# Kernel tuning notes

Measured on AMD Instinct MI355X. Metric: run time of the kernel, lower is better.

The kernel has to match this reference:

```python
import jax, jax.numpy as jnp
import numpy as np
import math

D_MODEL = 768
N_HEADS = 12
B, L = 2, 2048
ALPHA = 0.3

def setup_inputs() -> dict:
    key = jax.random.key(0)
    ks = jax.random.split(key, 7)
    s = 0.02
    return {
        "x": jax.random.normal(ks[0], (B, L, D_MODEL), dtype=jnp.float32),
        "Wqkv_w": jax.random.normal(ks[1], (D_MODEL, 3 * D_MODEL), dtype=jnp.float32) * s,
        "Wqkv_b": jax.random.normal(ks[2], (3 * D_MODEL,), dtype=jnp.float32) * s,
        "sel_w": jax.random.normal(ks[3], (D_MODEL, 2), dtype=jnp.float32) * s,
        "sel_b": jax.random.normal(ks[4], (2,), dtype=jnp.float32) * s,
        "out_w": jax.random.normal(ks[5], (D_MODEL, D_MODEL), dtype=jnp.float32) * s,
        "out_b": jax.random.normal(ks[6], (D_MODEL,), dtype=jnp.float32) * s,
        "temperature": jnp.ones((1,), dtype=jnp.float32) * (math.sqrt(D_MODEL) * ALPHA),
    }

def reference(x, Wqkv_w, Wqkv_b, sel_w, sel_b, out_w, out_b, temperature):
    b, l, d = x.shape
    h = N_HEADS
    hd = d // h
    # QKV projection: (B, L, 3, H, hd)
    qkv = (x @ Wqkv_w + Wqkv_b).reshape(b, l, 3, h, hd)
    q, k_, v = qkv[:, :, 0], qkv[:, :, 1], qkv[:, :, 2]
    scale = 1.0 / math.sqrt(hd)
    scores = jnp.einsum('bthd,bshd->bhts', q, k_ * scale)  # (B,H,L,L)
    causal_mask = jnp.triu(jnp.full((l, l), -10000.0, dtype=scores.dtype), 1)
    attn = jax.nn.softmax(scores + causal_mask, axis=-1)
    ctx = jnp.einsum('bhts,bshd->bthd', attn, v).reshape(b, l, d)
    attn_output = ctx @ out_w + out_b  # (B,L,D)
    # selection gate: softmax over 2 logits, keep prob of class 1 -> (B,L,1)
    selection = jax.nn.softmax((x @ sel_w + sel_b) / temperature, axis=-1)[..., 1:]
    # eval-mode top-k routing
    k_sel = int(math.ceil(math.sqrt(l)))
    _, idx = jax.lax.top_k(selection[..., 0], k_sel)  # (B, k)
    gated = attn_output * selection  # (B,L,D)
    src = jnp.take_along_axis(gated, idx[..., None], axis=1)  # (B,k,D)
    y = jax.vmap(lambda xb, ib, sb: xb.at[ib].add(sb))(x, idx, src)
    return y
```

## Files before the change

### kernel.cpp

```cpp
#include <hip/hip_runtime.h>
#include <hip/hip_bf16.h>
#include <cstddef>

#define BATCH 2
#define SEQ   2048
#define DM    768
#define NH    12
#define HD    64
#define N3    2304
#define NKV   1536
#define KSEL  46
#define NROW  (BATCH*KSEL)
#define NCHUNK 32

typedef unsigned short ushort_t;
typedef __attribute__((ext_vector_type(8))) short bf16x8;
typedef __attribute__((ext_vector_type(4))) float f32x4;

__device__ __forceinline__ ushort_t f2bf(float f) {
  union { __hip_bfloat16 h; ushort_t u; } cv;
  cv.h = __float2bfloat16(f);
  return cv.u;
}
__device__ __forceinline__ float bf2f(ushort_t u) {
  union { unsigned int i; float f; } cv;
  cv.i = ((unsigned int)u) << 16;
  return cv.f;
}

#define GLD16(g, l)                                                         \
  __builtin_amdgcn_global_load_lds(                                         \
      (const __attribute__((address_space(1))) void*)(g),                   \
      (__attribute__((address_space(3))) void*)(l), 16, 0, 0)

__global__ __launch_bounds__(256) void prep_kernel(
    const float* __restrict__ x, const float* __restrict__ W,
    const float* __restrict__ Wo,
    const float* __restrict__ sel_w, const float* __restrict__ sel_b,
    const float* __restrict__ temp,
    ushort_t* __restrict__ xb, ushort_t* __restrict__ Wt,
    ushort_t* __restrict__ WoT,
    float* __restrict__ sel, float* __restrict__ y) {
  const int bx = blockIdx.x;
  const int tid = threadIdx.x;
  if (bx < 1024) {
    const int w = tid >> 6, lane = tid & 63;
    const int row = bx * 4 + w;
    const float4* xr4 = (const float4*)(x + (size_t)row * DM);
    float4* yr4 = (float4*)(y + (size_t)row * DM);
    ushort4* xb4 = (ushort4*)(xb + (size_t)row * DM);
    const float4* sw4 = (const float4*)sel_w;
    float a0 = 0.f, a1 = 0.f;
#pragma unroll
    for (int i = 0; i < 3; ++i) {
      const int p = i * 64 + lane;
      float4 f = xr4[p];
      yr4[p] = f;
      ushort4 o;
      o.x = f2bf(f.x); o.y = f2bf(f.y); o.z = f2bf(f.z); o.w = f2bf(f.w);
      xb4[p] = o;
      float4 sa = sw4[p * 2];
      float4 sb = sw4[p * 2 + 1];
      a0 += f.x * sa.x + f.y * sa.z + f.z * sb.x + f.w * sb.z;
      a1 += f.x * sa.y + f.y * sa.w + f.z * sb.y + f.w * sb.w;
    }
    for (int off = 32; off; off >>= 1) {
      a0 += __shfl_xor(a0, off);
      a1 += __shfl_xor(a1, off);
    }
    if (lane == 0) {
      float t = temp[0];
      float l0 = (a0 + sel_b[0]) / t;
      float l1 = (a1 + sel_b[1]) / t;
      sel[row] = 1.0f / (1.0f + expf(l0 - l1));
    }
  } else if (bx < 2752) {
    __shared__ float tile[32][33];
    const int bx2 = bx - 1024;
    const int n0 = (bx2 % 72) * 32, k0 = (bx2 / 72) * 32;
    const int r = tid >> 3, c4 = (tid & 7) * 4;
    float4 f = *(const float4*)&W[(size_t)(k0 + r) * N3 + n0 + c4];
    tile[r][c4] = f.x; tile[r][c4 + 1] = f.y; tile[r][c4 + 2] = f.z; tile[r][c4 + 3] = f.w;
    __syncthreads();
    ushort4 o;
    o.x = f2bf(tile[c4 + 0][r]);
    o.y = f2bf(tile[c4 + 1][r]);
    o.z = f2bf(tile[c4 + 2][r]);
    o.w = f2bf(tile[c4 + 3][r]);
    *(ushort4*)&Wt[(size_t)(n0 + r) * DM + k0 + c4] = o;
  } else {
    __shared__ float tile2[32][33];
    const int bx3 = bx - 2752;
    const int n0 = (bx3 % 24) * 32, k0 = (bx3 / 24) * 32;
    const int r = tid >> 3, c4 = (tid & 7) * 4;
    float4 f = *(const float4*)&Wo[(size_t)(k0 + r) * DM + n0 + c4];
    tile2[r][c4] = f.x; tile2[r][c4 + 1] = f.y; tile2[r][c4 + 2] = f.z; tile2[r][c4 + 3] = f.w;
    __syncthreads();
    ushort4 o;
    o.x = f2bf(tile2[c4 + 0][r]);
    o.y = f2bf(tile2[c4 + 1][r]);
    o.z = f2bf(tile2[c4 + 2][r]);
    o.w = f2bf(tile2[c4 + 3][r]);
    *(ushort4*)&WoT[(size_t)(n0 + r) * DM + k0 + c4] = o;
  }
}

__global__ __launch_bounds__(256) void topk_kernel(
    const float* __restrict__ sel, int* __restrict__ idx,
    int* __restrict__ idxp) {
  __shared__ unsigned int hist[256];
  __shared__ unsigned int cum[256];
  __shared__ unsigned int wtot[4];
  __shared__ int sh_b;
  __shared__ int c_gt, c_eq;
  __shared__ int tmp_gt[KSEL];
  __shared__ int eqlist[256];
  const int b = blockIdx.x, tid = threadIdx.x;
  const int lane = tid & 63, w = tid >> 6;

  unsigned int key[8];
  int  kidx[8];
#pragma unroll
  for (int e = 0; e < 8; ++e) {
    int i = e * 256 + tid;
    kidx[e] = i;
    key[e] = __float_as_uint(sel[b * SEQ + i]);
  }
  unsigned int prefix = 0, mask = 0;
  int r = KSEL;
#pragma unroll
  for (int p = 3; p >= 0; --p) {
    const int shift = 8 * p;
    hist[tid] = 0;
    __syncthreads();
#pragma unroll
    for (int e = 0; e < 8; ++e)
      if ((key[e] & mask) == prefix)
        atomicAdd(&hist[(key[e] >> shift) & 255], 1u);
    __syncthreads();
    unsigned int v = hist[tid];
#pragma unroll
    for (int off = 1; off < 64; off <<= 1) {
      unsigned int t = __shfl_down(v, off);
      if (lane + off < 64) v += t;
    }
    if (lane == 0) wtot[w] = v;
    __syncthreads();
    unsigned int addhi = 0;
    for (int ww = w + 1; ww < 4; ++ww) addhi += wtot[ww];
    v += addhi;
    cum[tid] = v;
    __syncthreads();
    if (v >= (unsigned int)r && (tid == 255 || cum[tid + 1] < (unsigned int)r))
      sh_b = tid;
    __syncthreads();
    const int bsel = sh_b;
    r -= (bsel == 255) ? 0 : (int)cum[bsel + 1];
    prefix |= ((unsigned int)bsel) << shift;
    mask |= 0xFFu << shift;
    __syncthreads();
  }
  if (tid == 0) { c_gt = 0; c_eq = 0; }
  __syncthreads();
#pragma unroll
  for (int e = 0; e < 8; ++e) {
    if (key[e] > prefix) {
      int pos = atomicAdd(&c_gt, 1);
      tmp_gt[pos] = kidx[e];
    } else if (key[e] == prefix) {
      int pos = atomicAdd(&c_eq, 1);
      if (pos < 256) eqlist[pos] = kidx[e];
    }
  }
  __syncthreads();
  if (tid == 0) {
    const int need = KSEL - c_gt;
    const int ec = (c_eq < 256) ? c_eq : 256;
    for (int a = 0; a < need; ++a) {
      int mb = a;
      for (int bb = a + 1; bb < ec; ++bb)
        if (eqlist[bb] < eqlist[mb]) mb = bb;
      int tv = eqlist[a]; eqlist[a] = eqlist[mb]; eqlist[mb] = tv;
    }
  }
  __syncthreads();
  if (tid < 64) {
    if (tid < KSEL) {
      int t = (tid < c_gt) ? tmp_gt[tid] : eqlist[tid - c_gt];
      idx[b * KSEL + tid] = t;
      idxp[b * 64 + tid] = t;
    } else {
      idxp[b * 64 + tid] = 0;
    }
  }
}

__global__ __launch_bounds__(256) void gemm_kernel(
    const ushort_t* __restrict__ Xbf,
    const ushort_t* __restrict__ Wt,
    const float* __restrict__ bias,
    const int* __restrict__ idxp,
    ushort_t* __restrict__ Ckv,
    ushort_t* __restrict__ qb) {
  __shared__ ushort_t As[128 * 32];
  __shared__ ushort_t Bs[128 * 32];
  const int bid = blockIdx.x;
  const int tid = threadIdx.x;
  const int lane = tid & 63, w = tid >> 6;
  const int wr = w >> 1, wc = w & 1;
  const int quad = lane >> 4, l16 = lane & 15;
  const int ci0 = tid;
  const int ci1 = 256 + tid;
  const bool isQ = (bid >= 384);
  int m0, n0;
  size_t ga0, ga1;
  if (isQ) {
    m0 = 0;
    n0 = (bid - 384) * 128;
    const int r0 = ci0 >> 2, r1 = ci1 >> 2;
    ga0 = (size_t)((r0 >> 6) * SEQ + idxp[r0]) * DM;
    ga1 = (size_t)((r1 >> 6) * SEQ + idxp[r1]) * DM;
  } else {
    m0 = (bid / 12) * 128;
    n0 = 768 + (bid % 12) * 128;
    ga0 = (size_t)(m0 + (ci0 >> 2)) * DM;
    ga1 = (size_t)(m0 + (ci1 >> 2)) * DM;
  }
  const size_t gb0 = (size_t)(n0 + (ci0 >> 2)) * DM;
  const size_t gb1 = (size_t)(n0 + (ci1 >> 2)) * DM;
  const int ka0 = (ci0 & 3) * 8, ka1 = (ci1 & 3) * 8;

  f32x4 acc[4][4] = {};
  for (int k0 = 0; k0 < DM; k0 += 32) {
    GLD16(Xbf + ga0 + k0 + ka0, &As[(w * 64) * 8]);
    GLD16(Xbf + ga1 + k0 + ka1, &As[(256 + w * 64) * 8]);
    GLD16(Wt + gb0 + k0 + ka0, &Bs[(w * 64) * 8]);
    GLD16(Wt + gb1 + k0 + ka1, &Bs[(256 + w * 64) * 8]);
    __syncthreads();
    bf16x8 af[4], bfr[4];
#pragma unroll
    for (int i = 0; i < 4; ++i)
      af[i] = *(const bf16x8*)&As[(wr * 64 + i * 16 + l16) * 32 + quad * 8];
#pragma unroll
    for (int j = 0; j < 4; ++j)
      bfr[j] = *(const bf16x8*)&Bs[(wc * 64 + j * 16 + l16) * 32 + quad * 8];
#pragma unroll
    for (int i = 0; i < 4; ++i)
#pragma unroll
      for (int j = 0; j < 4; ++j)
        acc[i][j] = __builtin_amdgcn_mfma_f32_16x16x32_bf16(af[i], bfr[j], acc[i][j], 0, 0, 0);
    __syncthreads();
  }
#pragma unroll
  for (int i = 0; i < 4; ++i) {
    const int row_base = wr * 64 + i * 16 + quad * 4;
#pragma unroll
    for (int j = 0; j < 4; ++j) {
      const int col = n0 + wc * 64 + j * 16 + l16;
      const float bv = bias[col];
      if (isQ) {
#pragma unroll
        for (int r = 0; r < 4; ++r)
          qb[(size_t)(row_base + r) * DM + col] = f2bf(acc[i][j][r] + bv);
      } else {
#pragma unroll
        for (int r = 0; r < 4; ++r)
          Ckv[(size_t)(m0 + row_base + r) * NKV + (col - 768)] = f2bf(acc[i][j][r] + bv);
      }
    }
  }
}

__global__ __launch_bounds__(256) void attn_chunk_kernel(
    const ushort_t* __restrict__ kv,
    const ushort_t* __restrict__ qb,
    const int* __restrict__ idx,
    float* __restrict__ m_part, float* __restrict__ l_part,
    ushort_t* __restrict__ o_part) {
  __shared__ __align__(16) ushort_t Vt[64][72];
  __shared__ __align__(16) ushort_t Ps[4][16][72];
  __shared__ int tS[64];
  __shared__ int tmaxS;
  const int tid = threadIdx.x;
  const int c = blockIdx.x, h = blockIdx.y, b = blockIdx.z;
  const int c0 = c * 64;
  if (tid < 64) {
    int t = (tid < KSEL) ? idx[b * KSEL + tid] : -1;
    tS[tid] = t;
    int tm = t;
    for (int off = 32; off; off >>= 1) tm = max(tm, __shfl_xor(tm, off));
    if (tid == 0) tmaxS = tm;
  }
  __syncthreads();
  if (c0 > tmaxS) return;

  {
    const int key = tid >> 2, ds0 = (tid & 3) * 16;
    const ushort_t* vsrc = kv + (size_t)(b * SEQ + c0 + key) * NKV + DM + h * HD + ds0;
    ushort_t tmp[16];
    *(uint4*)&tmp[0] = *(const uint4*)&vsrc[0];
    *(uint4*)&tmp[8] = *(const uint4*)&vsrc[8];
#pragma unroll
    for (int i = 0; i < 16; ++i) Vt[ds0 + i][key] = tmp[i];
  }

  const int lane = tid & 63, w = tid >> 6;
  const int quad = lane >> 4, l16 = lane & 15;

  const ushort_t* qsrc = qb + (size_t)(b * 64 + w * 16 + l16) * DM + h * HD + quad * 8;
  bf16x8 aq0 = *(const bf16x8*)&qsrc[0];
  bf16x8 aq1 = *(const bf16x8*)&qsrc[32];

  f32x4 acc[4] = {};
#pragma unroll
  for (int nt = 0; nt < 4; ++nt) {
    const ushort_t* ksrc = kv + (size_t)(b * SEQ + c0 + nt * 16 + l16) * NKV + h * HD + quad * 8;
    bf16x8 bk0 = *(const bf16x8*)&ksrc[0];
    bf16x8 bk1 = *(const bf16x8*)&ksrc[32];
    acc[nt] = __builtin_amdgcn_mfma_f32_16x16x32_bf16(aq0, bk0, acc[nt], 0, 0, 0);
    acc[nt] = __builtin_amdgcn_mfma_f32_16x16x32_bf16(aq1, bk1, acc[nt], 0, 0, 0);
  }

  float p[4][4];
  float mrow[4], lrow[4];
#pragma unroll
  for (int r = 0; r < 4; ++r) {
    const int q = w * 16 + quad * 4 + r;
    const int t = tS[q];
    float mx = -1e30f;
#pragma unroll
    for (int nt = 0; nt < 4; ++nt) {
      float s = acc[nt][r] * 0.125f;
      if (c0 + nt * 16 + l16 > t) s = -1e30f;
      p[nt][r] = s;
      mx = fmaxf(mx, s);
    }
#pragma unroll
    for (int off = 1; off < 16; off <<= 1) mx = fmaxf(mx, __shfl_xor(mx, off));
    float sum = 0.f;
#pragma unroll
    for (int nt = 0; nt < 4; ++nt) {
      float pv = __expf(p[nt][r] - mx);
      p[nt][r] = pv;
      sum += pv;
    }
#pragma unroll
    for (int off = 1; off < 16; off <<= 1) sum += __shfl_xor(sum, off);
    mrow[r] = mx; lrow[r] = sum;
  }

  const size_t pbase = ((size_t)(b * NH + h) * NCHUNK + c) * 64;
  if (l16 == 0) {
#pragma unroll
    for (int r = 0; r < 4; ++r) {
      const int q = w * 16 + quad * 4 + r;
      m_part[pbase + q] = mrow[r];
      l_part[pbase + q] = lrow[r];
    }
  }

#pragma unroll
  for (int r = 0; r < 4; ++r)
#pragma unroll
    for (int nt = 0; nt < 4; ++nt)
      Ps[w][quad * 4 + r][nt * 16 + l16] = f2bf(p[nt][r]);
  __syncthreads();

  bf16x8 ap0 = *(const bf16x8*)&Ps[w][l16][quad * 8];
  bf16x8 ap1 = *(const bf16x8*)&Ps[w][l16][32 + quad * 8];
  f32x4 acc2[4] = {};
#pragma unroll
  for (int nt = 0; nt < 4; ++nt) {
    bf16x8 bv0 = *(const bf16x8*)&Vt[nt * 16 + l16][quad * 8];
    bf16x8 bv1 = *(const bf16x8*)&Vt[nt * 16 + l16][32 + quad * 8];
    acc2[nt] = __builtin_amdgcn_mfma_f32_16x16x32_bf16(ap0, bv0, acc2[nt], 0, 0, 0);
    acc2[nt] = __builtin_amdgcn_mfma_f32_16x16x32_bf16(ap1, bv1, acc2[nt], 0, 0, 0);
  }
  ushort_t* obp = o_part + pbase * 64;
#pragma unroll
  for (int nt = 0; nt < 4; ++nt)
#pragma unroll
    for (int r = 0; r < 4; ++r)
      obp[(w * 16 + quad * 4 + r) * 64 + nt * 16 + l16] = f2bf(acc2[nt][r]);
}

__global__ __launch_bounds__(256) void attn_combine_kernel(
    const float* __restrict__ m_part, const float* __restrict__ l_part,
    const ushort_t* __restrict__ o_part, const int* __restrict__ idx,
    ushort_t* __restrict__ ctx_bf) {
  __shared__ float wgt[NCHUNK][16];
  __shared__ float linv[16];
  __shared__ int ncS[16];
  const int rg = blockIdx.x, h = blockIdx.y, b = blockIdx.z;
  const int tid = threadIdx.x;
  const size_t base = (size_t)(b * NH + h) * NCHUNK * 64;
  if (tid < 16) {
    const int q = rg * 16 + tid;
    float L = 0.f; int nc = 0;
    if (q < KSEL) {
      const int t = idx[b * KSEL + q];
      nc = (t >> 6) + 1;
      float M = -1e30f;
      for (int cc = 0; cc < nc; ++cc)
        M = fmaxf(M, m_part[base + cc * 64 + q]);
      for (int cc = 0; cc < nc; ++cc) {
        float wv = __expf(m_part[base + cc * 64 + q] - M);
        wgt[cc][tid] = wv;
        L += wv * l_part[base + cc * 64 + q];
      }
    }
    ncS[tid] = nc;
    linv[tid] = (L > 0.f) ? 1.0f / L : 0.f;
  }
  __syncthreads();
  const int rl = tid >> 4;
  const int d4 = (tid & 15) * 4;
  const int q = rg * 16 + rl;
  if (q >= KSEL) return;
  const int nc = ncS[rl];
  float4 a = {0.f, 0.f, 0.f, 0.f};
  const ushort_t* obp = o_part + base * 64 + (size_t)q * 64 + d4;
  for (int cc = 0; cc < nc; ++cc) {
    const float wv = wgt[cc][rl];
    const ushort4 ov = *(const ushort4*)&obp[(size_t)cc * 4096];
    a.x += wv * bf2f(ov.x); a.y += wv * bf2f(ov.y);
    a.z += wv * bf2f(ov.z); a.w += wv * bf2f(ov.w);
  }
  const float li = linv[rl];
  ushort4 o;
  o.x = f2bf(a.x * li); o.y = f2bf(a.y * li);
  o.z = f2bf(a.z * li); o.w = f2bf(a.w * li);
  *(ushort4*)&ctx_bf[(size_t)(b * 64 + q) * DM + h * HD + d4] = o;
}

__global__ __launch_bounds__(256) void outproj_kernel(
    const ushort_t* __restrict__ ctx_bf,
    const ushort_t* __restrict__ WoT,
    const float* __restrict__ ob, const int* __restrict__ idx,
    const float* __restrict__ sel, float* __restrict__ y) {
  __shared__ ushort_t As[128 * 32];
  __shared__ ushort_t Bs[64 * 32];
  const int tid = threadIdx.x;
  const int lane = tid & 63, w = tid >> 6;
  const int wr = w >> 1, wc = w & 1;
  const int kb = blockIdx.x / 12;
  const int n0 = (blockIdx.x % 12) * 64;
  const int kbase = kb * 384;
  const int quad = lane >> 4, l16 = lane & 15;
  const int ci0 = tid;
  const int ci1 = 256 + tid;
  const size_t ga0 = (size_t)(ci0 >> 2) * DM;
  const size_t ga1 = (size_t)(ci1 >> 2) * DM;
  const size_t gb0 = (size_t)(n0 + (tid >> 2)) * DM;
  const int ka0 = (ci0 & 3) * 8, ka1 = (ci1 & 3) * 8;
  const int kq = (tid & 3) * 8;
  f32x4 acc[4][2] = {};
  for (int k0 = kbase; k0 < kbase + 384; k0 += 32) {
    GLD16(ctx_bf + ga0 + k0 + ka0, &As[(w * 64) * 8]);
    GLD16(ctx_bf + ga1 + k0 + ka1, &As[(256 + w * 64) * 8]);
    GLD16(WoT + gb0 + k0 + kq, &Bs[(w * 16) * 32]);
    __syncthreads();
    bf16x8 af[4], bfr[2];
#pragma unroll
    for (int i = 0; i < 4; ++i)
      af[i] = *(const bf16x8*)&As[(wr * 64 + i * 16 + l16) * 32 + quad * 8];
#pragma unroll
    for (int j = 0; j < 2; ++j)
      bfr[j] = *(const bf16x8*)&Bs[(wc * 32 + j * 16 + l16) * 32 + quad * 8];
#pragma unroll
    for (int i = 0; i < 4; ++i)
#pragma unroll
      for (int j = 0; j < 2; ++j)
        acc[i][j] = __builtin_amdgcn_mfma_f32_16x16x32_bf16(af[i], bfr[j], acc[i][j], 0, 0, 0);
    __syncthreads();
  }
#pragma unroll
  for (int i = 0; i < 4; ++i) {
#pragma unroll
    for (int r = 0; r < 4; ++r) {
      const int row = wr * 64 + i * 16 + quad * 4 + r;
      const int b = row >> 6, jj = row & 63;
      if (jj >= KSEL) continue;
      const int t = idx[b * KSEL + jj];
      const float sv = sel[b * SEQ + t];
      float* yr = y + (size_t)(b * SEQ + t) * DM;
#pragma unroll
      for (int j = 0; j < 2; ++j) {
        const int col = n0 + wc * 32 + j * 16 + l16;
        const float bv = (kb == 0) ? ob[col] : 0.f;
        atomicAdd(&yr[col], (acc[i][j][r] + bv) * sv);
      }
    }
  }
}

extern "C" void kernel_launch(void* const* d_in, const int* in_sizes, int n_in,
                              void* d_out, int out_size, void* d_ws, size_t ws_size,
                              hipStream_t stream) {
  const float* x      = (const float*)d_in[0];
  const float* Wqkv_w = (const float*)d_in[1];
  const float* Wqkv_b = (const float*)d_in[2];
  const float* sel_w  = (const float*)d_in[3];
  const float* sel_b  = (const float*)d_in[4];
  const float* out_w  = (const float*)d_in[5];
  const float* out_b  = (const float*)d_in[6];
  const float* temp   = (const float*)d_in[7];
  float* y = (float*)d_out;

  char* wsb = (char*)d_ws;
  ushort_t* kv     = (ushort_t*)wsb;  wsb += (size_t)BATCH * SEQ * NKV * 2;
  ushort_t* o_part = (ushort_t*)wsb;  wsb += (size_t)24 * NCHUNK * 64 * 64 * 2;
  float*    m_part = (float*)wsb;     wsb += (size_t)24 * NCHUNK * 64 * 4;
  float*    l_part = (float*)wsb;     wsb += (size_t)24 * NCHUNK * 64 * 4;
  float*    sel    = (float*)wsb;     wsb += (size_t)BATCH * SEQ * 4;
  int*      idx    = (int*)wsb;       wsb += 128 * 4;
  int*      idxp   = (int*)wsb;       wsb += 128 * 4;
  ushort_t* ctx_bf = (ushort_t*)wsb;  wsb += (size_t)128 * DM * 2;
  ushort_t* qb     = (ushort_t*)wsb;  wsb += (size_t)128 * DM * 2;
  ushort_t* Xbf    = (ushort_t*)wsb;  wsb += (size_t)BATCH * SEQ * DM * 2;
  ushort_t* Wt     = (ushort_t*)wsb;  wsb += (size_t)N3 * DM * 2;
  ushort_t* WoT    = (ushort_t*)wsb;  wsb += (size_t)DM * DM * 2;

  prep_kernel<<<dim3(3328), 256, 0, stream>>>(x, Wqkv_w, out_w, sel_w, sel_b, temp,
                                              Xbf, Wt, WoT, sel, y);
  topk_kernel<<<dim3(BATCH), 256, 0, stream>>>(sel, idx, idxp);
  gemm_kernel<<<dim3(390), 256, 0, stream>>>(Xbf, Wt, Wqkv_b, idxp, kv, qb);
  attn_chunk_kernel<<<dim3(NCHUNK, NH, BATCH), 256, 0, stream>>>(kv, qb, idx, m_part, l_part, o_part);
  attn_combine_kernel<<<dim3(3, NH, BATCH), 256, 0, stream>>>(m_part, l_part, o_part, idx, ctx_bf);
  outproj_kernel<<<dim3(24), 256, 0, stream>>>(ctx_bf, WoT, out_b, idx, sel, y);
}
```

Measured before the change: 154.8 us.

## Fuse top-k into Q-GEMM blocks and attention combine into chunk kernel

The separate top-k kernel is removed. Each of the six Q-projection GEMM blocks now recomputes the radix-select top-k for both batches itself and keeps the indices in shared memory, and block 384 writes idx for later kernels. The attention combine kernel is folded into the chunk kernel: a per-(batch,head) atomic counter, zeroed in the prep kernel, lets the last finishing chunk block merge the partial results. This removes two kernel launches and their serialization gaps, at the cost of redundant top-k work in the Q blocks, which delays them, and a serial combine tail run by one block per head.

```diff
diff --git a/kernel.cpp b/kernel.cpp
--- a/kernel.cpp
+++ b/kernel.cpp
@@ -40,10 +40,12 @@
     const float* __restrict__ temp,
     ushort_t* __restrict__ xb, ushort_t* __restrict__ Wt,
     ushort_t* __restrict__ WoT,
-    float* __restrict__ sel, float* __restrict__ y) {
+    float* __restrict__ sel, float* __restrict__ y,
+    unsigned int* __restrict__ cnt) {
   const int bx = blockIdx.x;
   const int tid = threadIdx.x;
   if (bx < 1024) {
+    if (bx == 0 && tid < NH * BATCH) cnt[tid] = 0u;
     const int w = tid >> 6, lane = tid & 63;
     const int row = bx * 4 + w;
     const float4* xr4 = (const float4*)(x + (size_t)row * DM);
@@ -105,105 +107,24 @@
   }
 }
 
-__global__ __launch_bounds__(256) void topk_kernel(
-    const float* __restrict__ sel, int* __restrict__ idx,
-    int* __restrict__ idxp) {
+__global__ __launch_bounds__(256) void gemm_kernel(
+    const ushort_t* __restrict__ Xbf,
+    const ushort_t* __restrict__ Wt,
+    const float* __restrict__ bias,
+    const float* __restrict__ sel,
+    int* __restrict__ idx,
+    ushort_t* __restrict__ Ckv,
+    ushort_t* __restrict__ qb) {
+  __shared__ ushort_t As[128 * 32];
+  __shared__ ushort_t Bs[128 * 32];
   __shared__ unsigned int hist[256];
-  __shared__ unsigned int cum[256];
+  __shared__ unsigned int cumS[256];
   __shared__ unsigned int wtot[4];
   __shared__ int sh_b;
   __shared__ int c_gt, c_eq;
   __shared__ int tmp_gt[KSEL];
   __shared__ int eqlist[256];
-  const int b = blockIdx.x, tid = threadIdx.x;
-  const int lane = tid & 63, w = tid >> 6;
-
-  unsigned int key[8];
-  int  kidx[8];
-#pragma unroll
-  for (int e = 0; e < 8; ++e) {
-    int i = e * 256 + tid;
-    kidx[e] = i;
-    key[e] = __float_as_uint(sel[b * SEQ + i]);
-  }
-  unsigned int prefix = 0, mask = 0;
-  int r = KSEL;
-#pragma unroll
-  for (int p = 3; p >= 0; --p) {
-    const int shift = 8 * p;
-    hist[tid] = 0;
-    __syncthreads();
-#pragma unroll
-    for (int e = 0; e < 8; ++e)
-      if ((key[e] & mask) == prefix)
-        atomicAdd(&hist[(key[e] >> shift) & 255], 1u);
-    __syncthreads();
-    unsigned int v = hist[tid];
-#pragma unroll
-    for (int off = 1; off < 64; off <<= 1) {
-      unsigned int t = __shfl_down(v, off);
-      if (lane + off < 64) v += t;
-    }
-    if (lane == 0) wtot[w] = v;
-    __syncthreads();
-    unsigned int addhi = 0;
-    for (int ww = w + 1; ww < 4; ++ww) addhi += wtot[ww];
-    v += addhi;
-    cum[tid] = v;
-    __syncthreads();
-    if (v >= (unsigned int)r && (tid == 255 || cum[tid + 1] < (unsigned int)r))
-      sh_b = tid;
-    __syncthreads();
-    const int bsel = sh_b;
-    r -= (bsel == 255) ? 0 : (int)cum[bsel + 1];
-    prefix |= ((unsigned int)bsel) << shift;
-    mask |= 0xFFu << shift;
-    __syncthreads();
-  }
-  if (tid == 0) { c_gt = 0; c_eq = 0; }
-  __syncthreads();
-#pragma unroll
-  for (int e = 0; e < 8; ++e) {
-    if (key[e] > prefix) {
-      int pos = atomicAdd(&c_gt, 1);
-      tmp_gt[pos] = kidx[e];
-    } else if (key[e] == prefix) {
-      int pos = atomicAdd(&c_eq, 1);
-      if (pos < 256) eqlist[pos] = kidx[e];
-    }
-  }
-  __syncthreads();
-  if (tid == 0) {
-    const int need = KSEL - c_gt;
-    const int ec = (c_eq < 256) ? c_eq : 256;
-    for (int a = 0; a < need; ++a) {
-      int mb = a;
-      for (int bb = a + 1; bb < ec; ++bb)
-        if (eqlist[bb] < eqlist[mb]) mb = bb;
-      int tv = eqlist[a]; eqlist[a] = eqlist[mb]; eqlist[mb] = tv;
-    }
-  }
-  __syncthreads();
-  if (tid < 64) {
-    if (tid < KSEL) {
-      int t = (tid < c_gt) ? tmp_gt[tid] : eqlist[tid - c_gt];
-      idx[b * KSEL + tid] = t;
-      idxp[b * 64 + tid] = t;
-    } else {
-      idxp[b * 64 + tid] = 0;
-    }
-  }
-}
-
-__global__ __launch_bounds__(256) void gemm_kernel(
-    const ushort_t* __restrict__ Xbf,
-    const ushort_t* __restrict__ Wt,
-    const float* __restrict__ bias,
-    const int* __restrict__ idxp,
-    ushort_t* __restrict__ Ckv,
-    ushort_t* __restrict__ qb) {
-  __shared__ ushort_t As[128 * 32];
-  __shared__ ushort_t Bs[128 * 32];
+  __shared__ int idxp_s[128];
   const int bid = blockIdx.x;
   const int tid = threadIdx.x;
   const int lane = tid & 63, w = tid >> 6;
@@ -215,11 +136,88 @@
   int m0, n0;
   size_t ga0, ga1;
   if (isQ) {
+    for (int bb = 0; bb < 2; ++bb) {
+      unsigned int key[8];
+      int kidx[8];
+#pragma unroll
+      for (int e = 0; e < 8; ++e) {
+        int i = e * 256 + tid;
+        kidx[e] = i;
+        key[e] = __float_as_uint(sel[bb * SEQ + i]);
+      }
+      unsigned int prefix = 0, msk = 0;
+      int rr = KSEL;
+#pragma unroll
+      for (int p = 3; p >= 0; --p) {
+        const int shift = 8 * p;
+        hist[tid] = 0;
+        __syncthreads();
+#pragma unroll
+        for (int e = 0; e < 8; ++e)
+          if ((key[e] & msk) == prefix)
+            atomicAdd(&hist[(key[e] >> shift) & 255], 1u);
+        __syncthreads();
+        unsigned int v = hist[tid];
+#pragma unroll
+        for (int off = 1; off < 64; off <<= 1) {
+          unsigned int t = __shfl_down(v, off);
+          if (lane + off < 64) v += t;
+        }
+        if (lane == 0) wtot[w] = v;
+        __syncthreads();
+        unsigned int addhi = 0;
+        for (int ww = w + 1; ww < 4; ++ww) addhi += wtot[ww];
+        v += addhi;
+        cumS[tid] = v;
+        __syncthreads();
+        if (v >= (unsigned int)rr && (tid == 255 || cumS[tid + 1] < (unsigned int)rr))
+          sh_b = tid;
+        __syncthreads();
+        const int bsel = sh_b;
+        rr -= (bsel == 255) ? 0 : (int)cumS[bsel + 1];
+        prefix |= ((unsigned int)bsel) << shift;
+        msk |= 0xFFu << shift;
+        __syncthreads();
+      }
+      if (tid == 0) { c_gt = 0; c_eq = 0; }
+      __syncthreads();
+#pragma unroll
+      for (int e = 0; e < 8; ++e) {
+        if (key[e] > prefix) {
+          int pos = atomicAdd(&c_gt, 1);
+          tmp_gt[pos] = kidx[e];
+        } else if (key[e] == prefix) {
+          int pos = atomicAdd(&c_eq, 1);
+          if (pos < 256) eqlist[pos] = kidx[e];
+        }
+      }
+      __syncthreads();
+      if (tid == 0) {
+        const int need = KSEL - c_gt;
+        const int ec = (c_eq < 256) ? c_eq : 256;
+        for (int a = 0; a < need; ++a) {
+          int mb = a;
+          for (int b2 = a + 1; b2 < ec; ++b2)
+            if (eqlist[b2] < eqlist[mb]) mb = b2;
+          int tv = eqlist[a]; eqlist[a] = eqlist[mb]; eqlist[mb] = tv;
+        }
+      }
+      __syncthreads();
+      if (tid < 64) {
+        int t = 0;
+        if (tid < KSEL) {
+          t = (tid < c_gt) ? tmp_gt[tid] : eqlist[tid - c_gt];
+          if (bid == 384) idx[bb * KSEL + tid] = t;
+        }
+        idxp_s[bb * 64 + tid] = t;
+      }
+      __syncthreads();
+    }
     m0 = 0;
     n0 = (bid - 384) * 128;
     const int r0 = ci0 >> 2, r1 = ci1 >> 2;
-    ga0 = (size_t)((r0 >> 6) * SEQ + idxp[r0]) * DM;
-    ga1 = (size_t)((r1 >> 6) * SEQ + idxp[r1]) * DM;
+    ga0 = (size_t)((r0 >> 6) * SEQ + idxp_s[r0]) * DM;
+    ga1 = (size_t)((r1 >> 6) * SEQ + idxp_s[r1]) * DM;
   } else {
     m0 = (bid / 12) * 128;
     n0 = 768 + (bid % 12) * 128;
@@ -276,11 +274,17 @@
     const ushort_t* __restrict__ qb,
     const int* __restrict__ idx,
     float* __restrict__ m_part, float* __restrict__ l_part,
-    ushort_t* __restrict__ o_part) {
+    ushort_t* __restrict__ o_part,
+    unsigned int* __restrict__ cnt,
+    ushort_t* __restrict__ ctx_bf) {
   __shared__ __align__(16) ushort_t Vt[64][72];
   __shared__ __align__(16) ushort_t Ps[4][16][72];
   __shared__ int tS[64];
   __shared__ int tmaxS;
+  __shared__ float wgt[NCHUNK][16];
+  __shared__ float linv[16];
+  __shared__ int ncS[16];
+  __shared__ unsigned int oldS;
   const int tid = threadIdx.x;
   const int c = blockIdx.x, h = blockIdx.y, b = blockIdx.z;
   const int c0 = c * 64;
@@ -292,145 +296,146 @@
     if (tid == 0) tmaxS = tm;
   }
   __syncthreads();
-  if (c0 > tmaxS) return;
-
-  {
-    const int key = tid >> 2, ds0 = (tid & 3) * 16;
-    const ushort_t* vsrc = kv + (size_t)(b * SEQ + c0 + key) * NKV + DM + h * HD + ds0;
-    ushort_t tmp[16];
-    *(uint4*)&tmp[0] = *(const uint4*)&vsrc[0];
-    *(uint4*)&tmp[8] = *(const uint4*)&vsrc[8];
-#pragma unroll
-    for (int i = 0; i < 16; ++i) Vt[ds0 + i][key] = tmp[i];
-  }
-
-  const int lane = tid & 63, w = tid >> 6;
-  const int quad = lane >> 4, l16 = lane & 15;
-
-  const ushort_t* qsrc = qb + (size_t)(b * 64 + w * 16 + l16) * DM + h * HD + quad * 8;
-  bf16x8 aq0 = *(const bf16x8*)&qsrc[0];
-  bf16x8 aq1 = *(const bf16x8*)&qsrc[32];
-
-  f32x4 acc[4] = {};
-#pragma unroll
-  for (int nt = 0; nt < 4; ++nt) {
-    const ushort_t* ksrc = kv + (size_t)(b * SEQ + c0 + nt * 16 + l16) * NKV + h * HD + quad * 8;
-    bf16x8 bk0 = *(const bf16x8*)&ksrc[0];
-    bf16x8 bk1 = *(const bf16x8*)&ksrc[32];
-    acc[nt] = __builtin_amdgcn_mfma_f32_16x16x32_bf16(aq0, bk0, acc[nt], 0, 0, 0);
-    acc[nt] = __builtin_amdgcn_mfma_f32_16x16x32_bf16(aq1, bk1, acc[nt], 0, 0, 0);
-  }
-
-  float p[4][4];
-  float mrow[4], lrow[4];
-#pragma unroll
-  for (int r = 0; r < 4; ++r) {
-    const int q = w * 16 + quad * 4 + r;
-    const int t = tS[q];
-    float mx = -1e30f;
+
+  if (c0 <= tmaxS) {
+    {
+      const int key = tid >> 2, ds0 = (tid & 3) * 16;
+      const ushort_t* vsrc = kv + (size_t)(b * SEQ + c0 + key) * NKV + DM + h * HD + ds0;
+      ushort_t tmp[16];
+      *(uint4*)&tmp[0] = *(const uint4*)&vsrc[0];
+      *(uint4*)&tmp[8] = *(const uint4*)&vsrc[8];
+#pragma unroll
+      for (int i = 0; i < 16; ++i) Vt[ds0 + i][key] = tmp[i];
+    }
+
+    const int lane = tid & 63, w = tid >> 6;
+    const int quad = lane >> 4, l16 = lane & 15;
+
+    const ushort_t* qsrc = qb + (size_t)(b * 64 + w * 16 + l16) * DM + h * HD + quad * 8;
+    bf16x8 aq0 = *(const bf16x8*)&qsrc[0];
+    bf16x8 aq1 = *(const bf16x8*)&qsrc[32];
+
+    f32x4 acc[4] = {};
 #pragma unroll
     for (int nt = 0; nt < 4; ++nt) {
-      float s = acc[nt][r] * 0.125f;
-      if (c0 + nt * 16 + l16 > t) s = -1e30f;
-      p[nt][r] = s;
-      mx = fmaxf(mx, s);
-    }
-#pragma unroll
-    for (int off = 1; off < 16; off <<= 1) mx = fmaxf(mx, __shfl_xor(mx, off));
-    float sum = 0.f;
-#pragma unroll
-    for (int nt = 0; nt < 4; ++nt) {
-      float pv = __expf(p[nt][r] - mx);
-      p[nt][r] = pv;
-      sum += pv;
-    }
-#pragma unroll
-    for (int off = 1; off < 16; off <<= 1) sum += __shfl_xor(sum, off);
-    mrow[r] = mx; lrow[r] = sum;
-  }
-
-  const size_t pbase = ((size_t)(b * NH + h) * NCHUNK + c) * 64;
-  if (l16 == 0) {
+      const ushort_t* ksrc = kv + (size_t)(b * SEQ + c0 + nt * 16 + l16) * NKV + h * HD + quad * 8;
+      bf16x8 bk0 = *(const bf16x8*)&ksrc[0];
+      bf16x8 bk1 = *(const bf16x8*)&ksrc[32];
+      acc[nt] = __builtin_amdgcn_mfma_f32_16x16x32_bf16(aq0, bk0, acc[nt], 0, 0, 0);
+      acc[nt] = __builtin_amdgcn_mfma_f32_16x16x32_bf16(aq1, bk1, acc[nt], 0, 0, 0);
+    }
+
+    float p[4][4];
+    float mrow[4], lrow[4];
 #pragma unroll
     for (int r = 0; r < 4; ++r) {
       const int q = w * 16 + quad * 4 + r;
-      m_part[pbase + q] = mrow[r];
-      l_part[pbase + q] = lrow[r];
-    }
-  }
-
-#pragma unroll
-  for (int r = 0; r < 4; ++r)
+      const int t = tS[q];
+      float mx = -1e30f;
+#pragma unroll
+      for (int nt = 0; nt < 4; ++nt) {
+        float s = acc[nt][r] * 0.125f;
+        if (c0 + nt * 16 + l16 > t) s = -1e30f;
+        p[nt][r] = s;
+        mx = fmaxf(mx, s);
+      }
+#pragma unroll
+      for (int off = 1; off < 16; off <<= 1) mx = fmaxf(mx, __shfl_xor(mx, off));
+      float sum = 0.f;
+#pragma unroll
+      for (int nt = 0; nt < 4; ++nt) {
+        float pv = __expf(p[nt][r] - mx);
+        p[nt][r] = pv;
+        sum += pv;
+      }
+#pragma unroll
+      for (int off = 1; off < 16; off <<= 1) sum += __shfl_xor(sum, off);
+      mrow[r] = mx; lrow[r] = sum;
+    }
+
+    const size_t pbase = ((size_t)(b * NH + h) * NCHUNK + c) * 64;
+    if (l16 == 0) {
+#pragma unroll
+      for (int r = 0; r < 4; ++r) {
+        const int q = w * 16 + quad * 4 + r;
+        m_part[pbase + q] = mrow[r];
+        l_part[pbase + q] = lrow[r];
+      }
+    }
+
+#pragma unroll
+    for (int r = 0; r < 4; ++r)
+#pragma unroll
+      for (int nt = 0; nt < 4; ++nt)
+        Ps[w][quad * 4 + r][nt * 16 + l16] = f2bf(p[nt][r]);
+    __syncthreads();
+
+    bf16x8 ap0 = *(const bf16x8*)&Ps[w][l16][quad * 8];
+    bf16x8 ap1 = *(const bf16x8*)&Ps[w][l16][32 + quad * 8];
+    f32x4 acc2[4] = {};
+#pragma unroll
+    for (int nt = 0; nt < 4; ++nt) {
+      bf16x8 bv0 = *(const bf16x8*)&Vt[nt * 16 + l16][quad * 8];
+      bf16x8 bv1 = *(const bf16x8*)&Vt[nt * 16 + l16][32 + quad * 8];
+      acc2[nt] = __builtin_amdgcn_mfma_f32_16x16x32_bf16(ap0, bv0, acc2[nt], 0, 0, 0);
+      acc2[nt] = __builtin_amdgcn_mfma_f32_16x16x32_bf16(ap1, bv1, acc2[nt], 0, 0, 0);
+    }
+    ushort_t* obp = o_part + pbase * 64;
 #pragma unroll
     for (int nt = 0; nt < 4; ++nt)
-      Ps[w][quad * 4 + r][nt * 16 + l16] = f2bf(p[nt][r]);
+#pragma unroll
+      for (int r = 0; r < 4; ++r)
+        obp[(w * 16 + quad * 4 + r) * 64 + nt * 16 + l16] = f2bf(acc2[nt][r]);
+  }
+
+  __threadfence();
+  if (tid == 0) oldS = atomicAdd(&cnt[b * NH + h], 1u);
   __syncthreads();
-
-  bf16x8 ap0 = *(const bf16x8*)&Ps[w][l16][quad * 8];
-  bf16x8 ap1 = *(const bf16x8*)&Ps[w][l16][32 + quad * 8];
-  f32x4 acc2[4] = {};
-#pragma unroll
-  for (int nt = 0; nt < 4; ++nt) {
-    bf16x8 bv0 = *(const bf16x8*)&Vt[nt * 16 + l16][quad * 8];
-    bf16x8 bv1 = *(const bf16x8*)&Vt[nt * 16 + l16][32 + quad * 8];
-    acc2[nt] = __builtin_amdgcn_mfma_f32_16x16x32_bf16(ap0, bv0, acc2[nt], 0, 0, 0);
-    acc2[nt] = __builtin_amdgcn_mfma_f32_16x16x32_bf16(ap1, bv1, acc2[nt], 0, 0, 0);
-  }
-  ushort_t* obp = o_part + pbase * 64;
-#pragma unroll
-  for (int nt = 0; nt < 4; ++nt)
-#pragma unroll
-    for (int r = 0; r < 4; ++r)
-      obp[(w * 16 + quad * 4 + r) * 64 + nt * 16 + l16] = f2bf(acc2[nt][r]);
-}
-
-__global__ __launch_bounds__(256) void attn_combine_kernel(
-    const float* __restrict__ m_part, const float* __restrict__ l_part,
-    const ushort_t* __restrict__ o_part, const int* __restrict__ idx,
-    ushort_t* __restrict__ ctx_bf) {
-  __shared__ float wgt[NCHUNK][16];
-  __shared__ float linv[16];
-  __shared__ int ncS[16];
-  const int rg = blockIdx.x, h = blockIdx.y, b = blockIdx.z;
-  const int tid = threadIdx.x;
-  const size_t base = (size_t)(b * NH + h) * NCHUNK * 64;
-  if (tid < 16) {
-    const int q = rg * 16 + tid;
-    float L = 0.f; int nc = 0;
-    if (q < KSEL) {
-      const int t = idx[b * KSEL + q];
-      nc = (t >> 6) + 1;
-      float M = -1e30f;
-      for (int cc = 0; cc < nc; ++cc)
-        M = fmaxf(M, m_part[base + cc * 64 + q]);
-      for (int cc = 0; cc < nc; ++cc) {
-        float wv = __expf(m_part[base + cc * 64 + q] - M);
-        wgt[cc][tid] = wv;
-        L += wv * l_part[base + cc * 64 + q];
-      }
-    }
-    ncS[tid] = nc;
-    linv[tid] = (L > 0.f) ? 1.0f / L : 0.f;
-  }
-  __syncthreads();
-  const int rl = tid >> 4;
-  const int d4 = (tid & 15) * 4;
-  const int q = rg * 16 + rl;
-  if (q >= KSEL) return;
-  const int nc = ncS[rl];
-  float4 a = {0.f, 0.f, 0.f, 0.f};
-  const ushort_t* obp = o_part + base * 64 + (size_t)q * 64 + d4;
-  for (int cc = 0; cc < nc; ++cc) {
-    const float wv = wgt[cc][rl];
-    const ushort4 ov = *(const ushort4*)&obp[(size_t)cc * 4096];
-    a.x += wv * bf2f(ov.x); a.y += wv * bf2f(ov.y);
-    a.z += wv * bf2f(ov.z); a.w += wv * bf2f(ov.w);
-  }
-  const float li = linv[rl];
-  ushort4 o;
-  o.x = f2bf(a.x * li); o.y = f2bf(a.y * li);
-  o.z = f2bf(a.z * li); o.w = f2bf(a.w * li);
-  *(ushort4*)&ctx_bf[(size_t)(b * 64 + q) * DM + h * HD + d4] = o;
+  if (oldS == NCHUNK - 1) {
+    __threadfence();
+    const size_t base = (size_t)(b * NH + h) * NCHUNK * 64;
+    for (int rg = 0; rg < 3; ++rg) {
+      if (tid < 16) {
+        const int q = rg * 16 + tid;
+        float L = 0.f; int nc = 0;
+        if (q < KSEL) {
+          const int t = idx[b * KSEL + q];
+          nc = (t >> 6) + 1;
+          float M = -1e30f;
+          for (int cc = 0; cc < nc; ++cc)
+            M = fmaxf(M, m_part[base + cc * 64 + q]);
+          for (int cc = 0; cc < nc; ++cc) {
+            float wv = __expf(m_part[base + cc * 64 + q] - M);
+            wgt[cc][tid] = wv;
+            L += wv * l_part[base + cc * 64 + q];
+          }
+        }
+        ncS[tid] = nc;
+        linv[tid] = (L > 0.f) ? 1.0f / L : 0.f;
+      }
+      __syncthreads();
+      const int rl = tid >> 4;
+      const int d4 = (tid & 15) * 4;
+      const int q = rg * 16 + rl;
+      if (q < KSEL) {
+        const int nc = ncS[rl];
+        float4 a = {0.f, 0.f, 0.f, 0.f};
+        const ushort_t* obp2 = o_part + base * 64 + (size_t)q * 64 + d4;
+        for (int cc = 0; cc < nc; ++cc) {
+          const float wv = wgt[cc][rl];
+          const ushort4 ov = *(const ushort4*)&obp2[(size_t)cc * 4096];
+          a.x += wv * bf2f(ov.x); a.y += wv * bf2f(ov.y);
+          a.z += wv * bf2f(ov.z); a.w += wv * bf2f(ov.w);
+        }
+        const float li = linv[rl];
+        ushort4 o;
+        o.x = f2bf(a.x * li); o.y = f2bf(a.y * li);
+        o.z = f2bf(a.z * li); o.w = f2bf(a.w * li);
+        *(ushort4*)&ctx_bf[(size_t)(b * 64 + q) * DM + h * HD + d4] = o;
+      }
+      __syncthreads();
+    }
+  }
 }
 
 __global__ __launch_bounds__(256) void outproj_kernel(
@@ -514,7 +519,7 @@
   float*    l_part = (float*)wsb;     wsb += (size_t)24 * NCHUNK * 64 * 4;
   float*    sel    = (float*)wsb;     wsb += (size_t)BATCH * SEQ * 4;
   int*      idx    = (int*)wsb;       wsb += 128 * 4;
-  int*      idxp   = (int*)wsb;       wsb += 128 * 4;
+  unsigned int* cnt = (unsigned int*)wsb; wsb += 128 * 4;
   ushort_t* ctx_bf = (ushort_t*)wsb;  wsb += (size_t)128 * DM * 2;
   ushort_t* qb     = (ushort_t*)wsb;  wsb += (size_t)128 * DM * 2;
   ushort_t* Xbf    = (ushort_t*)wsb;  wsb += (size_t)BATCH * SEQ * DM * 2;
@@ -522,10 +527,9 @@
   ushort_t* WoT    = (ushort_t*)wsb;  wsb += (size_t)DM * DM * 2;
 
   prep_kernel<<<dim3(3328), 256, 0, stream>>>(x, Wqkv_w, out_w, sel_w, sel_b, temp,
-                                              Xbf, Wt, WoT, sel, y);
-  topk_kernel<<<dim3(BATCH), 256, 0, stream>>>(sel, idx, idxp);
-  gemm_kernel<<<dim3(390), 256, 0, stream>>>(Xbf, Wt, Wqkv_b, idxp, kv, qb);
-  attn_chunk_kernel<<<dim3(NCHUNK, NH, BATCH), 256, 0, stream>>>(kv, qb, idx, m_part, l_part, o_part);
-  attn_combine_kernel<<<dim3(3, NH, BATCH), 256, 0, stream>>>(m_part, l_part, o_part, idx, ctx_bf);
-  outproj_kernel<<<dim3(24), 256, 0, stream>>>(ctx_bf, WoT, out_b, idx, sel, y);
-}
+                                              Xbf, Wt, WoT, sel, y, cnt);
+  gemm_kernel<<<dim3(390), 256, 0, stream>>>(Xbf, Wt, Wqkv_b, sel, idx, kv, qb);
+  attn_chunk_kernel<<<dim3(NCHUNK, NH, BATCH), 256, 0, stream>>>(kv, qb, idx, m_part, l_part,
+                                                                 o_part, cnt, ctx_bf);
+  outproj_kernel<<<dim3(6 * 4), 256, 0, stream>>>(ctx_bf, WoT, out_b, idx, sel, y);
+}
```

Result: slower. 267.8 us (+73.0%).

## Fuse K/V projection into attention chunks and sort top-k indices

Applied to the files above, without the earlier changes.

The K/V projection moves out of the big GEMM into the attention-chunk kernel. Each chunk block now computes its own 64-key K and V head slice from Xbf and Wt into shared memory, so the kv buffer no longer makes a round trip through global memory. Chunks past the largest selected index exit before doing any projection work, so K/V for unused tail positions is never computed. The top-k indices are also sorted, which makes the chunk cutoff depend on the maximum index. In exchange, each head block reloads its X tile, so X is read 12 times, and the per-block GEMM is small and uses only a single-wave-row layout.

```diff
diff --git a/kernel.cpp b/kernel.cpp
--- a/kernel.cpp
+++ b/kernel.cpp
@@ -115,6 +115,8 @@
   __shared__ int c_gt, c_eq;
   __shared__ int tmp_gt[KSEL];
   __shared__ int eqlist[256];
+  __shared__ int fin[64];
+  __shared__ int srt[64];
   const int b = blockIdx.x, tid = threadIdx.x;
   const int lane = tid & 63, w = tid >> 6;
 
@@ -184,50 +186,46 @@
     }
   }
   __syncthreads();
+  if (tid < KSEL)
+    fin[tid] = (tid < c_gt) ? tmp_gt[tid] : eqlist[tid - c_gt];
+  __syncthreads();
+  if (tid < KSEL) {
+    const int v = fin[tid];
+    int rank = 0;
+    for (int j = 0; j < KSEL; ++j) rank += (fin[j] < v);
+    srt[rank] = v;
+  }
+  __syncthreads();
   if (tid < 64) {
     if (tid < KSEL) {
-      int t = (tid < c_gt) ? tmp_gt[tid] : eqlist[tid - c_gt];
-      idx[b * KSEL + tid] = t;
-      idxp[b * 64 + tid] = t;
+      idx[b * KSEL + tid] = srt[tid];
+      idxp[b * 64 + tid] = srt[tid];
     } else {
       idxp[b * 64 + tid] = 0;
     }
   }
 }
 
-__global__ __launch_bounds__(256) void gemm_kernel(
+__global__ __launch_bounds__(256) void qgemm_kernel(
     const ushort_t* __restrict__ Xbf,
     const ushort_t* __restrict__ Wt,
     const float* __restrict__ bias,
     const int* __restrict__ idxp,
-    ushort_t* __restrict__ Ckv,
     ushort_t* __restrict__ qb) {
   __shared__ ushort_t As[128 * 32];
   __shared__ ushort_t Bs[128 * 32];
-  const int bid = blockIdx.x;
   const int tid = threadIdx.x;
   const int lane = tid & 63, w = tid >> 6;
   const int wr = w >> 1, wc = w & 1;
   const int quad = lane >> 4, l16 = lane & 15;
   const int ci0 = tid;
   const int ci1 = 256 + tid;
-  const bool isQ = (bid >= 384);
-  int m0, n0;
-  size_t ga0, ga1;
-  if (isQ) {
-    m0 = 0;
-    n0 = (bid - 384) * 128;
-    const int r0 = ci0 >> 2, r1 = ci1 >> 2;
-    ga0 = (size_t)((r0 >> 6) * SEQ + idxp[r0]) * DM;
-    ga1 = (size_t)((r1 >> 6) * SEQ + idxp[r1]) * DM;
-  } else {
-    m0 = (bid / 12) * 128;
-    n0 = 768 + (bid % 12) * 128;
-    ga0 = (size_t)(m0 + (ci0 >> 2)) * DM;
-    ga1 = (size_t)(m0 + (ci1 >> 2)) * DM;
-  }
-  const size_t gb0 = (size_t)(n0 + (ci0 >> 2)) * DM;
-  const size_t gb1 = (size_t)(n0 + (ci1 >> 2)) * DM;
+  const int n0 = blockIdx.x * 128;
+  const int r0 = ci0 >> 2, r1 = ci1 >> 2;
+  const size_t ga0 = (size_t)((r0 >> 6) * SEQ + idxp[r0]) * DM;
+  const size_t ga1 = (size_t)((r1 >> 6) * SEQ + idxp[r1]) * DM;
+  const size_t gb0 = (size_t)(n0 + r0) * DM;
+  const size_t gb1 = (size_t)(n0 + r1) * DM;
   const int ka0 = (ci0 & 3) * 8, ka1 = (ci1 & 3) * 8;
 
   f32x4 acc[4][4] = {};
@@ -258,25 +256,24 @@
     for (int j = 0; j < 4; ++j) {
       const int col = n0 + wc * 64 + j * 16 + l16;
       const float bv = bias[col];
-      if (isQ) {
-#pragma unroll
-        for (int r = 0; r < 4; ++r)
-          qb[(size_t)(row_base + r) * DM + col] = f2bf(acc[i][j][r] + bv);
-      } else {
-#pragma unroll
-        for (int r = 0; r < 4; ++r)
-          Ckv[(size_t)(m0 + row_base + r) * NKV + (col - 768)] = f2bf(acc[i][j][r] + bv);
-      }
+#pragma unroll
+      for (int r = 0; r < 4; ++r)
+        qb[(size_t)(row_base + r) * DM + col] = f2bf(acc[i][j][r] + bv);
     }
   }
 }
 
 __global__ __launch_bounds__(256) void attn_chunk_kernel(
-    const ushort_t* __restrict__ kv,
+    const ushort_t* __restrict__ Xbf,
+    const ushort_t* __restrict__ Wt,
+    const float* __restrict__ bias,
     const ushort_t* __restrict__ qb,
     const int* __restrict__ idx,
     float* __restrict__ m_part, float* __restrict__ l_part,
     ushort_t* __restrict__ o_part) {
+  __shared__ ushort_t As[64 * 32];
+  __shared__ ushort_t Bs[128 * 32];
+  __shared__ __align__(16) ushort_t Kc[64][72];
   __shared__ __align__(16) ushort_t Vt[64][72];
   __shared__ __align__(16) ushort_t Ps[4][16][72];
   __shared__ int tS[64];
@@ -294,18 +291,54 @@
   __syncthreads();
   if (c0 > tmaxS) return;
 
-  {
-    const int key = tid >> 2, ds0 = (tid & 3) * 16;
-    const ushort_t* vsrc = kv + (size_t)(b * SEQ + c0 + key) * NKV + DM + h * HD + ds0;
-    ushort_t tmp[16];
-    *(uint4*)&tmp[0] = *(const uint4*)&vsrc[0];
-    *(uint4*)&tmp[8] = *(const uint4*)&vsrc[8];
-#pragma unroll
-    for (int i = 0; i < 16; ++i) Vt[ds0 + i][key] = tmp[i];
-  }
-
   const int lane = tid & 63, w = tid >> 6;
   const int quad = lane >> 4, l16 = lane & 15;
+
+  const int arow = tid >> 2;
+  const int ka = (tid & 3) * 8;
+  const size_t gax = (size_t)(b * SEQ + c0 + arow) * DM;
+  const size_t gbk = (size_t)(768 + h * HD + arow) * DM;
+  const size_t gbv = (size_t)(1536 + h * HD + arow) * DM;
+
+  f32x4 accK[4] = {}, accV[4] = {};
+  for (int k0 = 0; k0 < DM; k0 += 32) {
+    GLD16(Xbf + gax + k0 + ka, &As[(w * 64) * 8]);
+    GLD16(Wt + gbk + k0 + ka, &Bs[(w * 64) * 8]);
+    GLD16(Wt + gbv + k0 + ka, &Bs[(256 + w * 64) * 8]);
+    __syncthreads();
+    bf16x8 aK = *(const bf16x8*)&Bs[(w * 16 + l16) * 32 + quad * 8];
+    bf16x8 aV = *(const bf16x8*)&As[(w * 16 + l16) * 32 + quad * 8];
+#pragma unroll
+    for (int j = 0; j < 4; ++j) {
+      bf16x8 bX = *(const bf16x8*)&As[(j * 16 + l16) * 32 + quad * 8];
+      bf16x8 bW = *(const bf16x8*)&Bs[(64 * 32) + (j * 16 + l16) * 32 + quad * 8];
+      accK[j] = __builtin_amdgcn_mfma_f32_16x16x32_bf16(aK, bX, accK[j], 0, 0, 0);
+      accV[j] = __builtin_amdgcn_mfma_f32_16x16x32_bf16(aV, bW, accV[j], 0, 0, 0);
+    }
+    __syncthreads();
+  }
+  {
+    float bK[4];
+#pragma unroll
+    for (int r = 0; r < 4; ++r) bK[r] = bias[768 + h * HD + w * 16 + quad * 4 + r];
+#pragma unroll
+    for (int j = 0; j < 4; ++j) {
+      ushort4 ok;
+      ok.x = f2bf(accK[j][0] + bK[0]);
+      ok.y = f2bf(accK[j][1] + bK[1]);
+      ok.z = f2bf(accK[j][2] + bK[2]);
+      ok.w = f2bf(accK[j][3] + bK[3]);
+      *(ushort4*)&Kc[j * 16 + l16][w * 16 + quad * 4] = ok;
+      const float bV = bias[1536 + h * HD + j * 16 + l16];
+      ushort4 ov;
+      ov.x = f2bf(accV[j][0] + bV);
+      ov.y = f2bf(accV[j][1] + bV);
+      ov.z = f2bf(accV[j][2] + bV);
+      ov.w = f2bf(accV[j][3] + bV);
+      *(ushort4*)&Vt[j * 16 + l16][w * 16 + quad * 4] = ov;
+    }
+  }
+  __syncthreads();
 
   const ushort_t* qsrc = qb + (size_t)(b * 64 + w * 16 + l16) * DM + h * HD + quad * 8;
   bf16x8 aq0 = *(const bf16x8*)&qsrc[0];
@@ -314,9 +347,8 @@
   f32x4 acc[4] = {};
 #pragma unroll
   for (int nt = 0; nt < 4; ++nt) {
-    const ushort_t* ksrc = kv + (size_t)(b * SEQ + c0 + nt * 16 + l16) * NKV + h * HD + quad * 8;
-    bf16x8 bk0 = *(const bf16x8*)&ksrc[0];
-    bf16x8 bk1 = *(const bf16x8*)&ksrc[32];
+    bf16x8 bk0 = *(const bf16x8*)&Kc[nt * 16 + l16][quad * 8];
+    bf16x8 bk1 = *(const bf16x8*)&Kc[nt * 16 + l16][32 + quad * 8];
     acc[nt] = __builtin_amdgcn_mfma_f32_16x16x32_bf16(aq0, bk0, acc[nt], 0, 0, 0);
     acc[nt] = __builtin_amdgcn_mfma_f32_16x16x32_bf16(aq1, bk1, acc[nt], 0, 0, 0);
   }
@@ -508,7 +540,6 @@
   float* y = (float*)d_out;
 
   char* wsb = (char*)d_ws;
-  ushort_t* kv     = (ushort_t*)wsb;  wsb += (size_t)BATCH * SEQ * NKV * 2;
   ushort_t* o_part = (ushort_t*)wsb;  wsb += (size_t)24 * NCHUNK * 64 * 64 * 2;
   float*    m_part = (float*)wsb;     wsb += (size_t)24 * NCHUNK * 64 * 4;
   float*    l_part = (float*)wsb;     wsb += (size_t)24 * NCHUNK * 64 * 4;
@@ -524,8 +555,9 @@
   prep_kernel<<<dim3(3328), 256, 0, stream>>>(x, Wqkv_w, out_w, sel_w, sel_b, temp,
                                               Xbf, Wt, WoT, sel, y);
   topk_kernel<<<dim3(BATCH), 256, 0, stream>>>(sel, idx, idxp);
-  gemm_kernel<<<dim3(390), 256, 0, stream>>>(Xbf, Wt, Wqkv_b, idxp, kv, qb);
-  attn_chunk_kernel<<<dim3(NCHUNK, NH, BATCH), 256, 0, stream>>>(kv, qb, idx, m_part, l_part, o_part);
+  qgemm_kernel<<<dim3(6), 256, 0, stream>>>(Xbf, Wt, Wqkv_b, idxp, qb);
+  attn_chunk_kernel<<<dim3(NCHUNK, NH, BATCH), 256, 0, stream>>>(Xbf, Wt, Wqkv_b, qb, idx,
+                                                                 m_part, l_part, o_part);
   attn_combine_kernel<<<dim3(3, NH, BATCH), 256, 0, stream>>>(m_part, l_part, o_part, idx, ctx_bf);
-  outproj_kernel<<<dim3(24), 256, 0, stream>>>(ctx_bf, WoT, out_b, idx, sel, y);
-}
+  outproj_kernel<<<dim3(6 * 4), 256, 0, stream>>>(ctx_bf, WoT, out_b, idx, sel, y);
+}
```

After: 163.6 us. +5.7%, slower.

## Halve QKV GEMM tile width, swizzle block order, and sort top-k indices

Applied to the files above, without the earlier changes.

The QKV projection GEMM changes from 128x128 tiles to 128x64 tiles. This doubles the grid from 390 to 780 blocks to fill more compute units, and halves per-block accumulator registers. K/V blocks are remapped with an XCD-style swizzle so neighbouring blocks share A rows in cache. The top-k kernel now sorts the selected indices ascending via a rank sort, which may improve locality of later gathers. The trade-off is more A-tile reloads across blocks and a little extra work in top-k.

```diff
diff --git a/kernel.cpp b/kernel.cpp
--- a/kernel.cpp
+++ b/kernel.cpp
@@ -115,6 +115,8 @@
   __shared__ int c_gt, c_eq;
   __shared__ int tmp_gt[KSEL];
   __shared__ int eqlist[256];
+  __shared__ int fin[64];
+  __shared__ int srt[64];
   const int b = blockIdx.x, tid = threadIdx.x;
   const int lane = tid & 63, w = tid >> 6;
 
@@ -184,11 +186,20 @@
     }
   }
   __syncthreads();
+  if (tid < KSEL)
+    fin[tid] = (tid < c_gt) ? tmp_gt[tid] : eqlist[tid - c_gt];
+  __syncthreads();
+  if (tid < KSEL) {
+    const int v = fin[tid];
+    int rank = 0;
+    for (int j = 0; j < KSEL; ++j) rank += (fin[j] < v);
+    srt[rank] = v;
+  }
+  __syncthreads();
   if (tid < 64) {
     if (tid < KSEL) {
-      int t = (tid < c_gt) ? tmp_gt[tid] : eqlist[tid - c_gt];
-      idx[b * KSEL + tid] = t;
-      idxp[b * 64 + tid] = t;
+      idx[b * KSEL + tid] = srt[tid];
+      idxp[b * 64 + tid] = srt[tid];
     } else {
       idxp[b * 64 + tid] = 0;
     }
@@ -203,7 +214,7 @@
     ushort_t* __restrict__ Ckv,
     ushort_t* __restrict__ qb) {
   __shared__ ushort_t As[128 * 32];
-  __shared__ ushort_t Bs[128 * 32];
+  __shared__ ushort_t Bs[64 * 32];
   const int bid = blockIdx.x;
   const int tid = threadIdx.x;
   const int lane = tid & 63, w = tid >> 6;
@@ -211,43 +222,43 @@
   const int quad = lane >> 4, l16 = lane & 15;
   const int ci0 = tid;
   const int ci1 = 256 + tid;
-  const bool isQ = (bid >= 384);
-  int m0, n0;
+  const bool isQ = (bid >= 768);
+  int m0, nw0;
   size_t ga0, ga1;
   if (isQ) {
     m0 = 0;
-    n0 = (bid - 384) * 128;
+    nw0 = (bid - 768) * 64;
     const int r0 = ci0 >> 2, r1 = ci1 >> 2;
     ga0 = (size_t)((r0 >> 6) * SEQ + idxp[r0]) * DM;
     ga1 = (size_t)((r1 >> 6) * SEQ + idxp[r1]) * DM;
   } else {
-    m0 = (bid / 12) * 128;
-    n0 = 768 + (bid % 12) * 128;
+    const int bid2 = (bid & 7) * 96 + (bid >> 3);
+    m0 = (bid2 / 24) * 128;
+    nw0 = 768 + (bid2 % 24) * 64;
     ga0 = (size_t)(m0 + (ci0 >> 2)) * DM;
     ga1 = (size_t)(m0 + (ci1 >> 2)) * DM;
   }
-  const size_t gb0 = (size_t)(n0 + (ci0 >> 2)) * DM;
-  const size_t gb1 = (size_t)(n0 + (ci1 >> 2)) * DM;
+  const size_t gb0 = (size_t)(nw0 + (tid >> 2)) * DM;
   const int ka0 = (ci0 & 3) * 8, ka1 = (ci1 & 3) * 8;
-
-  f32x4 acc[4][4] = {};
+  const int kq = (tid & 3) * 8;
+
+  f32x4 acc[4][2] = {};
   for (int k0 = 0; k0 < DM; k0 += 32) {
     GLD16(Xbf + ga0 + k0 + ka0, &As[(w * 64) * 8]);
     GLD16(Xbf + ga1 + k0 + ka1, &As[(256 + w * 64) * 8]);
-    GLD16(Wt + gb0 + k0 + ka0, &Bs[(w * 64) * 8]);
-    GLD16(Wt + gb1 + k0 + ka1, &Bs[(256 + w * 64) * 8]);
-    __syncthreads();
-    bf16x8 af[4], bfr[4];
+    GLD16(Wt + gb0 + k0 + kq, &Bs[(w * 16) * 32]);
+    __syncthreads();
+    bf16x8 af[4], bfr[2];
 #pragma unroll
     for (int i = 0; i < 4; ++i)
       af[i] = *(const bf16x8*)&As[(wr * 64 + i * 16 + l16) * 32 + quad * 8];
 #pragma unroll
-    for (int j = 0; j < 4; ++j)
-      bfr[j] = *(const bf16x8*)&Bs[(wc * 64 + j * 16 + l16) * 32 + quad * 8];
+    for (int j = 0; j < 2; ++j)
+      bfr[j] = *(const bf16x8*)&Bs[(wc * 32 + j * 16 + l16) * 32 + quad * 8];
 #pragma unroll
     for (int i = 0; i < 4; ++i)
 #pragma unroll
-      for (int j = 0; j < 4; ++j)
+      for (int j = 0; j < 2; ++j)
         acc[i][j] = __builtin_amdgcn_mfma_f32_16x16x32_bf16(af[i], bfr[j], acc[i][j], 0, 0, 0);
     __syncthreads();
   }
@@ -255,8 +266,8 @@
   for (int i = 0; i < 4; ++i) {
     const int row_base = wr * 64 + i * 16 + quad * 4;
 #pragma unroll
-    for (int j = 0; j < 4; ++j) {
-      const int col = n0 + wc * 64 + j * 16 + l16;
+    for (int j = 0; j < 2; ++j) {
+      const int col = nw0 + wc * 32 + j * 16 + l16;
       const float bv = bias[col];
       if (isQ) {
 #pragma unroll
@@ -524,8 +535,8 @@
   prep_kernel<<<dim3(3328), 256, 0, stream>>>(x, Wqkv_w, out_w, sel_w, sel_b, temp,
                                               Xbf, Wt, WoT, sel, y);
   topk_kernel<<<dim3(BATCH), 256, 0, stream>>>(sel, idx, idxp);
-  gemm_kernel<<<dim3(390), 256, 0, stream>>>(Xbf, Wt, Wqkv_b, idxp, kv, qb);
+  gemm_kernel<<<dim3(780), 256, 0, stream>>>(Xbf, Wt, Wqkv_b, idxp, kv, qb);
   attn_chunk_kernel<<<dim3(NCHUNK, NH, BATCH), 256, 0, stream>>>(kv, qb, idx, m_part, l_part, o_part);
   attn_combine_kernel<<<dim3(3, NH, BATCH), 256, 0, stream>>>(m_part, l_part, o_part, idx, ctx_bf);
-  outproj_kernel<<<dim3(24), 256, 0, stream>>>(ctx_bf, WoT, out_b, idx, sel, y);
-}
+  outproj_kernel<<<dim3(6 * 4), 256, 0, stream>>>(ctx_bf, WoT, out_b, idx, sel, y);
+}
```

After: 156.9 us. No clear change (+1.3%).
